# Kernel optimization log

Measured on AMD Instinct MI355X. Metric: run time of the kernel, lower is better.

Reference implementation:

```python
import jax, jax.numpy as jnp
import numpy as np

N_NODES = 100000
N_EDGES = 1600000
D = 64
N_LAYERS = 5  # hops=4 -> hops+1 GraphConv layers


def setup_inputs() -> dict:
    key = jax.random.key(0)
    k1, k2, k3, k4, k5, k6 = jax.random.split(key, 6)
    x = jax.random.normal(k1, (N_NODES, D), dtype=jnp.float32)
    edge_index = jax.random.randint(k2, (2, N_EDGES), 0, N_NODES, dtype=jnp.int64)
    edge_weight = jax.random.uniform(k3, (N_EDGES,), dtype=jnp.float32)
    # Per-layer params (all dims are 64 so we can stack): PyG GraphConv has
    # lin_rel (with bias) applied to the aggregated messages and lin_root
    # (no bias) applied to the node's own features.
    scale = 1.0 / np.sqrt(D)
    W_rel = jax.random.normal(k4, (N_LAYERS, D, D), dtype=jnp.float32) * scale
    b_rel = jnp.zeros((N_LAYERS, D), dtype=jnp.float32)
    W_root = jax.random.normal(k5, (N_LAYERS, D, D), dtype=jnp.float32) * scale
    return {"x": x, "edge_index": edge_index, "edge_weight": edge_weight,
            "W_rel": W_rel, "b_rel": b_rel, "W_root": W_root}


def _graph_conv(x, src, dst, edge_weight, W_rel_i, b_rel_i, W_root_i):
    # message: x_j * w_e ; aggregate: scatter-add onto destination nodes
    msg = x[src] * edge_weight[:, None]               # [E, D] gather
    agg = jax.ops.segment_sum(msg, dst, num_segments=N_NODES)  # [N, D] scatter
    return agg @ W_rel_i + b_rel_i + x @ W_root_i


def reference(x, edge_index, edge_weight, W_rel, b_rel, W_root):
    src, dst = edge_index[0], edge_index[1]
    h = x
    for i in range(N_LAYERS - 1):
        h = _graph_conv(h, src, dst, edge_weight, W_rel[i], b_rel[i], W_root[i])
        h = jax.nn.relu(h)
    h = _graph_conv(h, src, dst, edge_weight, W_rel[-1], b_rel[-1], W_root[-1])
    return h
```

## Files before the change

kernel.cpp:

```cpp
#include <hip/hip_runtime.h>

#define N_NODES 100000
#define N_EDGES 1600000
#define D 64
#define N_LAYERS 5
#define FB 1000
#define BN 100
#define NX 8
#define BCAP_X 320
#define BCAP 2048
#define BIN_BLOCKS 512
#define BIN_THREADS 512
#define BIN_CHUNK 3125

typedef unsigned short u16;
typedef unsigned long long u64;
typedef __attribute__((ext_vector_type(8))) short bf16x8;
typedef __attribute__((ext_vector_type(4))) float f32x4;

__device__ __forceinline__ float bf2f(u16 u) {
    union { unsigned int i; float f; } v;
    v.i = ((unsigned int)u) << 16;
    return v.f;
}
__device__ __forceinline__ u16 f2bf(float f) {
    union { float f; unsigned int i; } v;
    v.f = f;
    unsigned int r = v.i + 0x7FFFu + ((v.i >> 16) & 1u);
    return (u16)(r >> 16);
}
__device__ __forceinline__ float bf2f_lo(unsigned int pk) {
    union { unsigned int i; float f; } v;
    v.i = pk << 16;
    return v.f;
}
__device__ __forceinline__ float bf2f_hi(unsigned int pk) {
    union { unsigned int i; float f; } v;
    v.i = pk & 0xFFFF0000u;
    return v.f;
}


__global__ __launch_bounds__(1024) void initcur_kernel(int* __restrict__ fcur)
{
    int i = blockIdx.x * 1024 + threadIdx.x;
    if (i < NX * FB) fcur[i] = i * BCAP_X;
}

__global__ __launch_bounds__(BIN_THREADS) void bin_kernel(
    const int* __restrict__ src, const int* __restrict__ dst,
    const float* __restrict__ ew, int* __restrict__ fcur,
    u64* __restrict__ stag)
{
    __shared__ int hc[FB];
    const int xbase = (blockIdx.x & (NX - 1)) * FB;
    for (int b = threadIdx.x; b < FB; b += BIN_THREADS) hc[b] = 0;
    __syncthreads();
    const int e0 = blockIdx.x * BIN_CHUNK;
    for (int e = e0 + threadIdx.x; e < e0 + BIN_CHUNK; e += BIN_THREADS) {
        int d = dst[e];
        atomicAdd(&hc[d / BN], 1);
    }
    __syncthreads();
    for (int b = threadIdx.x; b < FB; b += BIN_THREADS) {
        int c = hc[b];
        if (c) hc[b] = atomicAdd(&fcur[xbase + b], c);
    }
    __syncthreads();
    for (int e = e0 + threadIdx.x; e < e0 + BIN_CHUNK; e += BIN_THREADS) {
        int d = dst[e];
        int b = d / BN;
        int pos = atomicAdd(&hc[b], 1);
        int s   = __builtin_nontemporal_load(&src[e]);
        float w = __builtin_nontemporal_load(&ew[e]);
        unsigned int pk = (unsigned int)((d - b * BN) << 17) | (unsigned int)s;
        u64 rec = ((u64)(unsigned int)__float_as_int(w) << 32) | pk;
        stag[pos] = rec;
    }
}

__global__ __launch_bounds__(1024) void fscan_kernel(
    const int* __restrict__ fcur, int* __restrict__ fbase,
    int* __restrict__ rowptr)
{
    __shared__ int s[1024];
    int t = threadIdx.x;
    int v = 0;
    if (t < FB) {
        #pragma unroll
        for (int x = 0; x < NX; ++x) {
            int cell = x * FB + t;
            v += fcur[cell] - cell * BCAP_X;
        }
    }
    s[t] = v;
    __syncthreads();
    for (int off = 1; off < 1024; off <<= 1) {
        int u = (t >= off) ? s[t - off] : 0;
        __syncthreads();
        s[t] += u;
        __syncthreads();
    }
    if (t < FB) fbase[t] = s[t] - v;
    if (t == FB - 1) {
        fbase[FB] = s[t];
        rowptr[N_NODES] = s[t];
    }
}

__global__ __launch_bounds__(256) void sort_kernel(
    const u64* __restrict__ stag, const int* __restrict__ fcur,
    const int* __restrict__ fbase, int* __restrict__ rowptr,
    int2* __restrict__ edges)
{
    __shared__ u64 ls[BCAP];
    __shared__ int cnt[BN];
    __shared__ int cur[BN];
    __shared__ int sc[128];
    const int b = blockIdx.x;
    const int base = fbase[b];
    const int t = threadIdx.x;
    for (int i = t; i < BN; i += 256) cnt[i] = 0;
    __syncthreads();
    int ofs = 0;
    #pragma unroll
    for (int x = 0; x < NX; ++x) {
        int cell = x * FB + b;
        int sz = fcur[cell] - cell * BCAP_X;
        const u64* sp = stag + (size_t)cell * BCAP_X;
        for (int i = t; i < sz; i += 256) {
            u64 r = __builtin_nontemporal_load(&sp[i]);
            ls[ofs + i] = r;
            atomicAdd(&cnt[((unsigned int)r) >> 17], 1);
        }
        ofs += sz;
    }
    const int size = ofs;
    __syncthreads();
    if (t < 128) sc[t] = (t < BN) ? cnt[t] : 0;
    __syncthreads();
    for (int off = 1; off < 128; off <<= 1) {
        int u = 0;
        if (t < 128 && t >= off) u = sc[t - off];
        __syncthreads();
        if (t < 128) sc[t] += u;
        __syncthreads();
    }
    if (t < BN) {
        int excl = sc[t] - cnt[t];
        rowptr[b * BN + t] = base + excl;
        cur[t] = excl;
    }
    __syncthreads();
    for (int i = t; i < size; i += 256) {
        u64 r = ls[i];
        unsigned int lo = (unsigned int)r;
        int dloc = lo >> 17;
        int rank = atomicAdd(&cur[dloc], 1);
        edges[base + rank] = make_int2((int)(lo & 0x1FFFFu),
                                       (int)(unsigned int)(r >> 32));
    }
}

__global__ __launch_bounds__(256) void f2bf_kernel(
    const float* __restrict__ in, u16* __restrict__ out)
{
    int i = blockIdx.x * 256 + threadIdx.x;
    if (i >= (N_NODES * D) / 4) return;
    float4 v = ((const float4*)in)[i];
    ushort4 o;
    o.x = f2bf(v.x); o.y = f2bf(v.y); o.z = f2bf(v.z); o.w = f2bf(v.w);
    ((ushort4*)out)[i] = o;
}

__global__ __launch_bounds__(256) void wprep_kernel(
    const float* __restrict__ Wrel, const float* __restrict__ Wroot,
    u16* __restrict__ W2T)
{
    int i = blockIdx.x * 256 + threadIdx.x;
    if (i >= N_LAYERS * 64 * 128) return;
    int l = i / (64 * 128);
    int rem = i % (64 * 128);
    int n = rem >> 7;
    int k = rem & 127;
    float v = (k < 64) ? Wrel[l * 4096 + k * 64 + n]
                       : Wroot[l * 4096 + (k - 64) * 64 + n];
    W2T[i] = f2bf(v);
}

__global__ __launch_bounds__(1024) void layer_kernel(
    const u16* __restrict__ hin, const int* __restrict__ rowptr,
    const int2* __restrict__ edges, const u16* __restrict__ W2T,
    const float* __restrict__ brel,
    u16* __restrict__ hout_bf, float* __restrict__ hout_f32, int relu)
{
    __shared__ u16 aggs[16][64];
    const int wave = threadIdx.x >> 6;
    const int lane = threadIdx.x & 63;
    const int nb16 = blockIdx.x * 16;
    const int sl   = lane & 31;
    const int eo   = lane >> 5;

    {
        const int node = nb16 + wave;
        const int b = __builtin_amdgcn_readfirstlane(rowptr[node]);
        const int e = __builtin_amdgcn_readfirstlane(rowptr[node + 1]);
        const u64* eseg = (const u64*)edges;
        float acc0 = 0.f, acc1 = 0.f;
        int j = b;

        #define PAIR(ra, rb) {                                               \
            int   s_ = (int)(unsigned int)(eo ? (rb) : (ra));                \
            float w_ = __int_as_float((int)(unsigned int)                    \
                                      ((eo ? (rb) : (ra)) >> 32));           \
            unsigned int p_ = *(const unsigned int*)                         \
                              (hin + ((size_t)s_ << 6) + sl * 2);            \
            acc0 += bf2f_lo(p_) * w_;                                        \
            acc1 += bf2f_hi(p_) * w_; }

        for (; j + 8 <= e; j += 8) {
            u64 r0 = eseg[j + 0], r1 = eseg[j + 1];
            u64 r2 = eseg[j + 2], r3 = eseg[j + 3];
            u64 r4 = eseg[j + 4], r5 = eseg[j + 5];
            u64 r6 = eseg[j + 6], r7 = eseg[j + 7];
            PAIR(r0, r1); PAIR(r2, r3); PAIR(r4, r5); PAIR(r6, r7);
        }
        for (; j + 2 <= e; j += 2) {
            u64 ra = eseg[j], rb = eseg[j + 1];
            PAIR(ra, rb);
        }
        if (j < e) {
            u64 ra = eseg[j];
            if (eo == 0) {
                int   s_ = (int)(unsigned int)ra;
                float w_ = __int_as_float((int)(unsigned int)(ra >> 32));
                unsigned int p_ = *(const unsigned int*)
                                  (hin + ((size_t)s_ << 6) + sl * 2);
                acc0 += bf2f_lo(p_) * w_;
                acc1 += bf2f_hi(p_) * w_;
            }
        }
        #undef PAIR

        acc0 += __shfl_xor(acc0, 32);
        acc1 += __shfl_xor(acc1, 32);
        if (eo == 0) {
            int u16idx = (wave << 6) | ((sl * 2) ^ ((wave & 7) << 3));
            unsigned int o = ((unsigned int)f2bf(acc1) << 16) | f2bf(acc0);
            *(unsigned int*)(&aggs[0][0] + u16idx) = o;
        }
    }
    __syncthreads();

    if (wave < 4) {
        const int nt = wave;
        const int m = lane & 15;
        const int q = lane >> 4;

        bf16x8 a[4];
        {
            int r0 = (m << 6) | ((q * 8) ^ ((m & 7) << 3));
            int r1 = (m << 6) | ((32 + q * 8) ^ ((m & 7) << 3));
            a[0] = *(const bf16x8*)(&aggs[0][0] + r0);
            a[1] = *(const bf16x8*)(&aggs[0][0] + r1);
        }
        size_t rowa = (size_t)(nb16 + m) << 6;
        a[2] = *(const bf16x8*)(hin + rowa + q * 8);
        a[3] = *(const bf16x8*)(hin + rowa + 32 + q * 8);

        bf16x8 bfr[4];
        #pragma unroll
        for (int kk = 0; kk < 4; ++kk)
            bfr[kk] = *(const bf16x8*)(W2T + (size_t)(nt * 16 + m) * 128
                                       + kk * 32 + q * 8);

        float bv = brel[nt * 16 + m];
        f32x4 acc = (f32x4){bv, bv, bv, bv};
        #pragma unroll
        for (int kk = 0; kk < 4; ++kk)
            acc = __builtin_amdgcn_mfma_f32_16x16x32_bf16(a[kk], bfr[kk],
                                                          acc, 0, 0, 0);

        #pragma unroll
        for (int r = 0; r < 4; ++r) {
            int n2 = nb16 + q * 4 + r;
            float v = acc[r];
            if (relu) v = fmaxf(v, 0.f);
            int dim = nt * 16 + m;
            if (hout_f32) hout_f32[(size_t)n2 * 64 + dim] = v;
            else          hout_bf [(size_t)n2 * 64 + dim] = f2bf(v);
        }
    }
}

extern "C" void kernel_launch(void* const* d_in, const int* in_sizes, int n_in,
                              void* d_out, int out_size, void* d_ws, size_t ws_size,
                              hipStream_t stream)
{
    const float* x     = (const float*)d_in[0];
    const int*   ei    = (const int*)d_in[1];
    const float* ew    = (const float*)d_in[2];
    const float* Wrel  = (const float*)d_in[3];
    const float* brel  = (const float*)d_in[4];
    const float* Wroot = (const float*)d_in[5];
    float* out = (float*)d_out;

    const int* src = ei;
    const int* dst = ei + N_EDGES;

    const size_t featb_bytes = (size_t)N_NODES * D * 2;
    char* ws = (char*)d_ws;
    size_t off = 0;
    u16*  hb     = (u16*)(ws + off);  off += featb_bytes;
    u16*  hb2    = (u16*)(ws + off);  off += featb_bytes;
    u16*  W2T    = (u16*)(ws + off);  off += (size_t)N_LAYERS * 64 * 128 * 2;
    int*  rowptr = (int*)(ws + off);  off += 400016;
    int*  fcur   = (int*)(ws + off);  off += NX * FB * 4;
    int*  fbase  = (int*)(ws + off);  off += (FB + 1) * 4 + 60;
    int2* edges  = (int2*)(ws + off); off += (size_t)N_EDGES * 8;

    u64* stag = (u64*)ws;

    u16* hbuf[2] = {hb, hb2};

    const int cblocks = (N_NODES * D / 4 + 255) / 256;
    const int wblocks = (N_LAYERS * 64 * 128 + 255) / 256;
    const int lblocks = N_NODES / 16;

    initcur_kernel<<<8, 1024, 0, stream>>>(fcur);
    bin_kernel<<<BIN_BLOCKS, BIN_THREADS, 0, stream>>>(src, dst, ew, fcur, stag);
    fscan_kernel<<<1, 1024, 0, stream>>>(fcur, fbase, rowptr);
    sort_kernel<<<FB, 256, 0, stream>>>(stag, fcur, fbase, rowptr, edges);
    f2bf_kernel<<<cblocks, 256, 0, stream>>>(x, hb);
    wprep_kernel<<<wblocks, 256, 0, stream>>>(Wrel, Wroot, W2T);

    for (int layer = 0; layer < N_LAYERS; ++layer) {
        int last = (layer == N_LAYERS - 1);
        layer_kernel<<<lblocks, 1024, 0, stream>>>(
            hbuf[layer & 1], rowptr, edges,
            W2T + (size_t)layer * 64 * 128,
            brel + (size_t)layer * D,
            last ? nullptr : hbuf[(layer + 1) & 1],
            last ? out : nullptr,
            last ? 0 : 1);
    }
}
```

Baseline: 447.9 us.

## Restructure aggregation: two nodes per wave with 16-byte row gathers

Each wave now aggregates two destination nodes instead of one. Each lane loads a 16-byte slice of a neighbour's bf16 row, and eight edges are processed in parallel across lane groups, with the first 32 edges per node issued up front to raise memory-level parallelism. Block size drops from 1024 to 512 threads with an occupancy hint of 4 blocks per CU, and a butterfly shuffle reduction combines the per-group partial sums. This trades more registers and extra shuffle reductions for wider, more numerous outstanding gathers, aiming to hide gather latency better.

After: 390.4 us. 1.15x faster.

```diff
diff --git a/kernel.cpp b/kernel.cpp
--- a/kernel.cpp
+++ b/kernel.cpp
@@ -188,7 +188,21 @@
     W2T[i] = f2bf(v);
 }
 
-__global__ __launch_bounds__(1024) void layer_kernel(
+#define GDECL2(N) uint4 N##h; float N##w
+#define GLOAD2(N, bb, ee, gg) {                                             \
+    int  ei_ = (bb) + (gg) * 8 + g8;                                        \
+    bool v_  = ei_ < (ee);                                                  \
+    int2 r_  = edges[v_ ? ei_ : 0];                                         \
+    N##w = v_ ? __int_as_float(r_.y) : 0.f;                                 \
+    int  s_  = v_ ? r_.x : 0;                                               \
+    N##h = *(const uint4*)(hin + ((size_t)s_ << 6) + (size_t)k * 8); }
+#define GCONS2(N, A) {                                                      \
+    A[0] += bf2f_lo(N##h.x) * N##w;  A[1] += bf2f_hi(N##h.x) * N##w;        \
+    A[2] += bf2f_lo(N##h.y) * N##w;  A[3] += bf2f_hi(N##h.y) * N##w;        \
+    A[4] += bf2f_lo(N##h.z) * N##w;  A[5] += bf2f_hi(N##h.z) * N##w;        \
+    A[6] += bf2f_lo(N##h.w) * N##w;  A[7] += bf2f_hi(N##h.w) * N##w; }
+
+__global__ __launch_bounds__(512, 4) void layer_kernel(
     const u16* __restrict__ hin, const int* __restrict__ rowptr,
     const int2* __restrict__ edges, const u16* __restrict__ W2T,
     const float* __restrict__ brel,
@@ -198,56 +212,65 @@
     const int wave = threadIdx.x >> 6;
     const int lane = threadIdx.x & 63;
     const int nb16 = blockIdx.x * 16;
-    const int sl   = lane & 31;
-    const int eo   = lane >> 5;
+    const int k    = lane & 7;
+    const int g8   = lane >> 3;
 
     {
-        const int node = nb16 + wave;
-        const int b = __builtin_amdgcn_readfirstlane(rowptr[node]);
-        const int e = __builtin_amdgcn_readfirstlane(rowptr[node + 1]);
-        const u64* eseg = (const u64*)edges;
-        float acc0 = 0.f, acc1 = 0.f;
-        int j = b;
-
-        #define PAIR(ra, rb) {                                               \
-            int   s_ = (int)(unsigned int)(eo ? (rb) : (ra));                \
-            float w_ = __int_as_float((int)(unsigned int)                    \
-                                      ((eo ? (rb) : (ra)) >> 32));           \
-            unsigned int p_ = *(const unsigned int*)                         \
-                              (hin + ((size_t)s_ << 6) + sl * 2);            \
-            acc0 += bf2f_lo(p_) * w_;                                        \
-            acc1 += bf2f_hi(p_) * w_; }
-
-        for (; j + 8 <= e; j += 8) {
-            u64 r0 = eseg[j + 0], r1 = eseg[j + 1];
-            u64 r2 = eseg[j + 2], r3 = eseg[j + 3];
-            u64 r4 = eseg[j + 4], r5 = eseg[j + 5];
-            u64 r6 = eseg[j + 6], r7 = eseg[j + 7];
-            PAIR(r0, r1); PAIR(r2, r3); PAIR(r4, r5); PAIR(r6, r7);
-        }
-        for (; j + 2 <= e; j += 2) {
-            u64 ra = eseg[j], rb = eseg[j + 1];
-            PAIR(ra, rb);
-        }
-        if (j < e) {
-            u64 ra = eseg[j];
-            if (eo == 0) {
-                int   s_ = (int)(unsigned int)ra;
-                float w_ = __int_as_float((int)(unsigned int)(ra >> 32));
-                unsigned int p_ = *(const unsigned int*)
-                                  (hin + ((size_t)s_ << 6) + sl * 2);
-                acc0 += bf2f_lo(p_) * w_;
-                acc1 += bf2f_hi(p_) * w_;
+        const int n0 = nb16 + 2 * wave;
+        const int b0 = rowptr[n0];
+        const int b1 = rowptr[n0 + 1];
+        const int e1 = rowptr[n0 + 2];
+        const int ng0 = (b1 - b0 + 7) >> 3;
+        const int ng1 = (e1 - b1 + 7) >> 3;
+
+        float a0[8], a1[8];
+        #pragma unroll
+        for (int i = 0; i < 8; ++i) { a0[i] = 0.f; a1[i] = 0.f; }
+
+        GDECL2(p0); GDECL2(p1); GDECL2(p2); GDECL2(p3);
+        GDECL2(q0); GDECL2(q1); GDECL2(q2); GDECL2(q3);
+        GLOAD2(p0, b0, b1, 0); GLOAD2(q0, b1, e1, 0);
+        GLOAD2(p1, b0, b1, 1); GLOAD2(q1, b1, e1, 1);
+        GLOAD2(p2, b0, b1, 2); GLOAD2(q2, b1, e1, 2);
+        GLOAD2(p3, b0, b1, 3); GLOAD2(q3, b1, e1, 3);
+        GCONS2(p0, a0); GCONS2(q0, a1);
+        GCONS2(p1, a0); GCONS2(q1, a1);
+        if (ng0 > 2) GCONS2(p2, a0);
+        if (ng1 > 2) GCONS2(q2, a1);
+        if (ng0 > 3) GCONS2(p3, a0);
+        if (ng1 > 3) GCONS2(q3, a1);
+        if (ng0 > 4)
+            for (int g = 4; g < ng0; ++g) {
+                GDECL2(t); GLOAD2(t, b0, b1, g); GCONS2(t, a0);
             }
-        }
-        #undef PAIR
-
-        acc0 += __shfl_xor(acc0, 32);
-        acc1 += __shfl_xor(acc1, 32);
-        if (eo == 0) {
-            int u16idx = (wave << 6) | ((sl * 2) ^ ((wave & 7) << 3));
-            unsigned int o = ((unsigned int)f2bf(acc1) << 16) | f2bf(acc0);
-            *(unsigned int*)(&aggs[0][0] + u16idx) = o;
+        if (ng1 > 4)
+            for (int g = 4; g < ng1; ++g) {
+                GDECL2(u); GLOAD2(u, b1, e1, g); GCONS2(u, a1);
+            }
+
+        #pragma unroll
+        for (int i = 0; i < 8; ++i) {
+            a0[i] += __shfl_xor(a0[i], 8);
+            a0[i] += __shfl_xor(a0[i], 16);
+            a0[i] += __shfl_xor(a0[i], 32);
+            a1[i] += __shfl_xor(a1[i], 8);
+            a1[i] += __shfl_xor(a1[i], 16);
+            a1[i] += __shfl_xor(a1[i], 32);
+        }
+
+        if (lane < 16) {
+            int which = lane >> 3;
+            int nl = 2 * wave + which;
+            unsigned int pk[4];
+            #pragma unroll
+            for (int d = 0; d < 4; ++d) {
+                float lo = which ? a1[2 * d]     : a0[2 * d];
+                float hi = which ? a1[2 * d + 1] : a0[2 * d + 1];
+                pk[d] = ((unsigned int)f2bf(hi) << 16) | f2bf(lo);
+            }
+            int off = (nl << 6) + ((8 * k) ^ ((nl & 7) << 3));
+            *(uint4*)(&aggs[0][0] + off) = make_uint4(pk[0], pk[1],
+                                                      pk[2], pk[3]);
         }
     }
     __syncthreads();
@@ -336,7 +359,7 @@
 
     for (int layer = 0; layer < N_LAYERS; ++layer) {
         int last = (layer == N_LAYERS - 1);
-        layer_kernel<<<lblocks, 1024, 0, stream>>>(
+        layer_kernel<<<lblocks, 512, 0, stream>>>(
             hbuf[layer & 1], rowptr, edges,
             W2T + (size_t)layer * 64 * 128,
             brel + (size_t)layer * D,
```
